# Kernel optimization log

Measured on AMD Instinct MI355X. Metric: run time of the kernel, lower is better.

The kernel has to match this reference:

```python
import jax, jax.numpy as jnp
import numpy as np

H = 64   # hid_dim (hard-coded in Attn_LSTM)
C = 8    # enc_in / out_dim
L = 96   # enc_seq_len = interval*lag = max_length
T = 24   # pre_len = window*horizon
B = 4096


def _p(key, shape, scale=0.1):
    return (jax.random.normal(key, shape, dtype=jnp.float32) * scale)


def setup_inputs() -> dict:
    key = jax.random.key(0)
    ks = jax.random.split(key, 20)
    inp = {
        'x_enc': jax.random.normal(ks[0], (B, L, C), dtype=jnp.float32),
        'x_mark_enc': jax.random.normal(ks[1], (B, L, 4), dtype=jnp.float32),
        'x_dec': jax.random.normal(ks[2], (B, T, C), dtype=jnp.float32),
        'x_mark_dec': jax.random.normal(ks[3], (B, T, 4), dtype=jnp.float32),
        # encoder LSTM (1 layer, input C -> hid H), pytorch gate order i,f,g,o
        'enc_Wih': _p(ks[4], (4 * H, C)), 'enc_Whh': _p(ks[5], (4 * H, H)),
        'enc_bih': _p(ks[6], (4 * H,)), 'enc_bhh': _p(ks[7], (4 * H,)),
        # decoder
        'emb_W': _p(ks[8], (H, C)), 'emb_b': _p(ks[9], (H,)),
        'attn_W': _p(ks[10], (L, 2 * H)), 'attn_b': _p(ks[11], (L,)),
        'comb_W': _p(ks[12], (H, 2 * H)), 'comb_b': _p(ks[13], (H,)),
        'dec_Wih': _p(ks[14], (4 * H, H)), 'dec_Whh': _p(ks[15], (4 * H, H)),
        'dec_bih': _p(ks[16], (4 * H,)), 'dec_bhh': _p(ks[17], (4 * H,)),
        'out_W': _p(ks[18], (C, H)), 'out_b': _p(ks[19], (C,)),
    }
    return inp


def _lstm_cell(x, h, c, Wih, Whh, bih, bhh):
    g = x @ Wih.T + h @ Whh.T + (bih + bhh)
    i, f, gg, o = jnp.split(g, 4, axis=-1)
    i, f, o = jax.nn.sigmoid(i), jax.nn.sigmoid(f), jax.nn.sigmoid(o)
    c_new = f * c + i * jnp.tanh(gg)
    h_new = o * jnp.tanh(c_new)
    return h_new, c_new


def _forward(x_enc, enc_Wih, enc_Whh, enc_bih, enc_bhh,
             emb_W, emb_b, attn_W, attn_b, comb_W, comb_b,
             dec_Wih, dec_Whh, dec_bih, dec_bhh, out_W, out_b):
    seq_last = x_enc[:, -1:, :]               # [B,1,C]
    x = x_enc - seq_last                      # normalized

    # ---- encoder: 1-layer LSTM over L steps ----
    h0 = jnp.zeros((x.shape[0], H), dtype=x.dtype)
    c0 = jnp.zeros_like(h0)

    def enc_step(carry, xt):
        h, c = carry
        h, c = _lstm_cell(xt, h, c, enc_Wih, enc_Whh, enc_bih, enc_bhh)
        return (h, c), h

    (h_enc, c_enc), enc_out = jax.lax.scan(enc_step, (h0, c0),
                                           jnp.swapaxes(x, 0, 1))
    enc_out = jnp.swapaxes(enc_out, 0, 1)     # [B,L,H]

    # ---- attention decoder: T sequential steps ----
    dec_in0 = x[:, -1, :]                     # last (normalized) input, [B,C]

    def dec_step(carry, _):
        inp, h, c = carry
        emb = jax.nn.relu(inp @ emb_W.T + emb_b)                       # [B,H]
        aw = jax.nn.softmax(jnp.concatenate([emb, h], -1) @ attn_W.T + attn_b)  # [B,L]
        ctx = jnp.einsum('bl,blh->bh', aw, enc_out)                    # [B,H]
        comb = jnp.concatenate([emb, ctx], -1) @ comb_W.T + comb_b     # [B,H]
        h, c = _lstm_cell(comb, h, c, dec_Wih, dec_Whh, dec_bih, dec_bhh)
        pred = h @ out_W.T + out_b                                     # [B,C]
        # original code feeds prediction.detach() back in
        return (jax.lax.stop_gradient(pred), h, c), (pred, aw)

    _, (preds, aws) = jax.lax.scan(dec_step, (dec_in0, h_enc, c_enc),
                                   None, length=T)
    pre_y = jnp.swapaxes(preds, 0, 1) + seq_last   # [B,T,C]
    return pre_y


def reference(x_enc, x_mark_enc, x_dec, x_mark_dec,
              enc_Wih, enc_Whh, enc_bih, enc_bhh,
              emb_W, emb_b, attn_W, attn_b, comb_W, comb_b,
              dec_Wih, dec_Whh, dec_bih, dec_bhh, out_W, out_b):
    # x_mark_enc, x_dec, x_mark_dec are accepted but unused (as in original)
    return _forward(x_enc, enc_Wih, enc_Whh, enc_bih, enc_bhh,
                    emb_W, emb_b, attn_W, attn_b, comb_W, comb_b,
                    dec_Wih, dec_Whh, dec_bih, dec_bhh, out_W, out_b)
```

## Files before the change

kernel.cpp:

```cpp
#include <hip/hip_runtime.h>

#define LL 96
#define TT 24
#define HH 64
#define CC 8
#define GG 256
#define BT 8
#define NB 512

typedef unsigned short u16t;
typedef unsigned int   u32t;
typedef __attribute__((ext_vector_type(8))) short bf16x8;
typedef __attribute__((ext_vector_type(4))) float f32x4;

__device__ __forceinline__ float b2f(u16t u){ union{u32t i; float f;} v; v.i=((u32t)u)<<16; return v.f; }
__device__ __forceinline__ float lo2f(u32t p){ union{u32t i; float f;} v; v.i=p<<16; return v.f; }
__device__ __forceinline__ float hi2f(u32t p){ union{u32t i; float f;} v; v.i=p&0xffff0000u; return v.f; }
__device__ __forceinline__ u16t f2b(float f){ union{float f; u32t i;} v; v.f=f; u32t l=(v.i>>16)&1u; v.i+=0x7fffu+l; return (u16t)(v.i>>16); }
__device__ __forceinline__ float rcpf(float x){ return __builtin_amdgcn_rcpf(x); }
__device__ __forceinline__ float sigm(float x){ return rcpf(1.f + __expf(-x)); }
__device__ __forceinline__ float tanh2(float x){ return 1.f - 2.f*rcpf(__expf(2.f*x) + 1.f); }
__device__ __forceinline__ u32t pk2(float a, float b){ return (u32t)f2b(a) | ((u32t)f2b(b)<<16); }
__device__ __forceinline__ bf16x8 u2b8(uint4 u){ union{uint4 a; bf16x8 b;} v; v.a=u; return v.b; }
__device__ __forceinline__ int aaddr(int k, int m){ return (((k>>5)*4 + ((k>>3)&3))*16 + m)*8 + (k&7); }

template<bool F32> __device__ __forceinline__ float ldf(const void* p, size_t i){
    if constexpr (F32) return ((const float*)p)[i];
    else               return b2f(((const u16t*)p)[i]);
}
template<bool F32> __device__ __forceinline__ uint4 ld8p(const void* p, size_t i){
    if constexpr (F32){
        const float* f = (const float*)p + i;
        uint4 r; r.x = pk2(f[0],f[1]); r.y = pk2(f[2],f[3]);
                 r.z = pk2(f[4],f[5]); r.w = pk2(f[6],f[7]);
        return r;
    } else return *(const uint4*)((const u16t*)p + i);
}
template<bool F32> __device__ __forceinline__ void stf(void* p, size_t i, float v){
    if constexpr (F32) ((float*)p)[i] = v;
    else               ((u16t*)p)[i] = f2b(v);
}
template<bool F32> __device__ __forceinline__ float ldW_enc(const void* wih, const void* whh, int r, int k){
    if (k < CC)      return ldf<F32>(wih, (size_t)r*CC + k);
    else if (k < 72) return ldf<F32>(whh, (size_t)r*HH + (k-CC));
    else             return 0.f;
}

__device__ __forceinline__ bool inputs_are_f32(const void* bih){
    const u16t* p = (const u16t*)bih;
    int cnt = 0;
    #pragma unroll
    for (int i = 0; i < 64; ++i){
        u32t e = ((u32t)p[i] >> 7) & 0xFFu;
        cnt += (e >= 128u) ? 1 : 0;
    }
    return cnt > 0;
}

template<bool F32>
__global__ __launch_bounds__(256,4) void enc4_g(
    const void* __restrict__ x_enc,
    const void* __restrict__ eWih, const void* __restrict__ eWhh,
    const void* __restrict__ ebih, const void* __restrict__ ebhh,
    u16t* __restrict__ eoG, float* __restrict__ cG)
{
    if (inputs_are_f32(ebih) != F32) return;

    __shared__ __align__(16) short Abuf2[2][1536];

    const int tid = threadIdx.x;
    const int b0  = blockIdx.x * 4;
    const int col = tid & 15, quad = (tid >> 4) & 3, wv = tid >> 6;

    bf16x8 Bf[4][3];
    float  biasg[4];
    #pragma unroll
    for (int g = 0; g < 4; ++g){
        int r = g*64 + wv*16 + col;
        biasg[g] = ldf<F32>(ebih, r) + ldf<F32>(ebhh, r);
        #pragma unroll
        for (int kb = 0; kb < 3; ++kb){
            bf16x8 v;
            #pragma unroll
            for (int x = 0; x < 8; ++x){
                int k = kb*32 + quad*8 + x;
                v[x] = (short)f2b(ldW_enc<F32>(eWih, eWhh, r, k));
            }
            Bf[g][kb] = v;
        }
    }
    for (int n = tid; n < 2*1536; n += 256) ((short*)Abuf2)[n] = 0;
    float sl = 0.f; size_t xbase = 0;
    if (tid < 32){ int b = tid >> 3, i = tid & 7;
        xbase = (size_t)(b0+b)*(LL*CC) + i;
        sl = ldf<F32>(x_enc, xbase + (size_t)(LL-1)*CC);
    }
    __syncthreads();
    if (tid < 32){ short v = (short)f2b(ldf<F32>(x_enc, xbase) - sl);
        Abuf2[0][tid] = v; Abuf2[0][tid+32] = v; Abuf2[0][tid+64] = v; Abuf2[0][tid+96] = v; }
    float xr = (tid < 32) ? ldf<F32>(x_enc, xbase + CC) : 0.f;

    const int jmy = wv*16 + col;
    const int hwbase = aaddr(8 + jmy, 0);
    const u32t ebase = ((u32t)(b0 + quad)*4u + (u32t)(jmy>>4))*1536u + (u32t)((jmy&15)*8);

    float creg = 0.f;
    u32t  pkv  = 0;

    #pragma unroll 2
    for (int t = 0; t < LL; ++t){
        __syncthreads();
        const bf16x8* AbR = (const bf16x8*)Abuf2[t & 1];
        short*        AbW = Abuf2[(t + 1) & 1];
        bf16x8 a0 = AbR[(0*4 + quad)*16 + col];
        bf16x8 a1 = AbR[(1*4 + quad)*16 + col];
        bf16x8 a2 = AbR[(2*4 + quad)*16 + col];
        f32x4 acc[4];
        #pragma unroll
        for (int g = 0; g < 4; ++g){
            f32x4 a; a[0]=biasg[g]; a[1]=biasg[g]; a[2]=biasg[g]; a[3]=biasg[g];
            a = __builtin_amdgcn_mfma_f32_16x16x32_bf16(a0, Bf[g][0], a, 0,0,0);
            a = __builtin_amdgcn_mfma_f32_16x16x32_bf16(a1, Bf[g][1], a, 0,0,0);
            a = __builtin_amdgcn_mfma_f32_16x16x32_bf16(a2, Bf[g][2], a, 0,0,0);
            acc[g] = a;
        }
        float c = sigm(acc[1][quad])*creg + sigm(acc[0][quad])*tanh2(acc[2][quad]);
        float h = sigm(acc[3][quad])*tanh2(c);
        creg = c;
        u16t hb = f2b(h);
        if ((t & 1) == 0) pkv = hb;
        else {
            pkv |= ((u32t)hb) << 16;
            *(u32t*)&eoG[ebase + (u32t)((t>>5)*512 + ((t>>3)&3)*128 + (t&7) - 1)] = pkv;
        }
        AbW[hwbase + quad*8]      = (short)hb;
        AbW[hwbase + quad*8+32]   = (short)hb;
        AbW[hwbase + quad*8+64]   = (short)hb;
        AbW[hwbase + quad*8+96]   = (short)hb;
        if (tid < 32 && t < LL-1){
            short v = (short)f2b(xr - sl);
            AbW[tid] = v; AbW[tid+32] = v; AbW[tid+64] = v; AbW[tid+96] = v;
            int tn = (t+2 < LL) ? t+2 : LL-1;
            xr = ldf<F32>(x_enc, xbase + (size_t)tn*CC);
        }
    }
    cG[(size_t)(b0 + quad)*HH + jmy] = creg;
}

template<bool F32>
__global__ __launch_bounds__(256,2) void dec8_g(
    const void* __restrict__ x_enc,
    const void* __restrict__ embW, const void* __restrict__ embb,
    const void* __restrict__ attnW, const void* __restrict__ attnb,
    const void* __restrict__ combW, const void* __restrict__ combb,
    const void* __restrict__ dWih, const void* __restrict__ dWhh,
    const void* __restrict__ dbih, const void* __restrict__ dbhh,
    const void* __restrict__ outW, const void* __restrict__ outb,
    void* __restrict__ outp, const u16t* __restrict__ eoG,
    const float* __restrict__ cG)
{
    if (inputs_are_f32(dbih) != F32) return;

    __shared__ __align__(16) float slp[CC*10];
    __shared__ __align__(16) char  uni[18880];

    const int tid = threadIdx.x;
    const int b0  = blockIdx.x * BT;
    const int col = tid & 15, quad = (tid >> 4) & 3, wv = tid >> 6;
    const int r0  = (quad >> 1) * 2;
    const int jmy = wv*16 + col;

    if (tid < BT*CC){ int b = tid >> 3, i = tid & 7;
        slp[i*10 + b] = ldf<F32>(x_enc, (size_t)(b0+b)*(LL*CC) + (size_t)(LL-1)*CC + i); }

    bf16x8 Bd[4][4];
    #pragma unroll
    for (int g = 0; g < 4; ++g){
        int r = g*64 + wv*16 + col;
        Bd[g][0] = u2b8(ld8p<F32>(dWih, (size_t)r*HH + quad*8));
        Bd[g][1] = u2b8(ld8p<F32>(dWih, (size_t)r*HH + 32 + quad*8));
        Bd[g][2] = u2b8(ld8p<F32>(dWhh, (size_t)r*HH + quad*8));
        Bd[g][3] = u2b8(ld8p<F32>(dWhh, (size_t)r*HH + 32 + quad*8));
    }
    bf16x8 Ba[2][4];
    #pragma unroll
    for (int kb = 0; kb < 4; ++kb)
        Ba[0][kb] = u2b8(ld8p<F32>(attnW, (size_t)(wv*16+col)*128 + kb*32 + quad*8));
    if (wv < 2){
        #pragma unroll
        for (int kb = 0; kb < 4; ++kb)
            Ba[1][kb] = u2b8(ld8p<F32>(attnW, (size_t)((4+wv)*16+col)*128 + kb*32 + quad*8));
    } else {
        #pragma unroll
        for (int kb = 0; kb < 4; ++kb) Ba[1][kb] = Ba[0][kb];
    }
    bf16x8 Bc[4];
    #pragma unroll
    for (int kb = 0; kb < 4; ++kb)
        Bc[kb] = u2b8(ld8p<F32>(combW, (size_t)(wv*16+col)*128 + kb*32 + quad*8));
    bf16x8 zz = {0,0,0,0,0,0,0,0};
    bf16x8 eBf = zz;
    if (quad == 0) eBf = u2b8(ld8p<F32>(embW, (size_t)(wv*16+col)*CC));
    bf16x8 oBf0 = zz, oBf1 = zz;
    if (col < CC){
        oBf0 = u2b8(ld8p<F32>(outW, (size_t)col*HH + quad*8));
        oBf1 = u2b8(ld8p<F32>(outW, (size_t)col*HH + 32 + quad*8));
    }

    float* decB  = (float*)(uni + 0);
    float* attnB = (float*)(uni + 1024);
    float* embB  = (float*)(uni + 1408);
    float* combB = (float*)(uni + 1664);
    float* outB  = (float*)(uni + 1920);
    float* Lg    = (float*)(uni + 1952);
    u16t*  awB   = (u16t*)(uni + 5024);
    u16t*  Ae    = (u16t*)(uni + 6560);
    u16t*  Ah0   = (u16t*)(uni + 8608);
    u16t*  Ah1   = (u16t*)(uni + 10656);
    u16t*  Actx  = (u16t*)(uni + 12704);
    u16t*  Acmb  = (u16t*)(uni + 14752);
    u16t*  Apred = (u16t*)(uni + 16800);

    float creg[2];
    #pragma unroll
    for (int rr = 0; rr < 2; ++rr){
        int b = (quad*4 + r0 + rr) & 7;
        u16t hv = eoG[(((size_t)(b0+b)*4 + (size_t)(jmy>>4))*3 + 2)*512 + 3*128 + (jmy&15)*8 + 7];
        Ah0[aaddr(jmy, b)]   = hv;
        Ah0[aaddr(jmy, b+8)] = hv;
        creg[rr] = cG[(size_t)(b0+b)*HH + jmy];
    }
    decB[tid] = ldf<F32>(dbih, tid) + ldf<F32>(dbhh, tid);
    if (tid < LL) attnB[tid] = ldf<F32>(attnb, tid);
    if (tid < HH) embB[tid]  = ldf<F32>(embb, tid);
    if (tid < HH) combB[tid] = ldf<F32>(combb, tid);
    if (tid < CC) outB[tid]  = ldf<F32>(outb, tid);
    for (int n = tid; n < 1024; n += 256) Apred[n] = 0;
    __syncthreads();

    const u16t* ebp = eoG + (size_t)(b0 + wv*2) * 6144;
    uint4 eF0[12], eF1[12];
    #pragma unroll
    for (int f = 0; f < 12; ++f) eF0[f] = *(const uint4*)(ebp + f*512 + quad*128 + col*8);
    #pragma unroll
    for (int f = 0; f < 12; ++f) eF1[f] = *(const uint4*)(ebp + 6144 + f*512 + quad*128 + col*8);

    const int lgS = tid & 31, bS = tid >> 5;
    const bf16x8* AeV   = (const bf16x8*)Ae;
    const bf16x8* ActxV = (const bf16x8*)Actx;
    const bf16x8* AcmbV = (const bf16x8*)Acmb;
    const bf16x8* ApV   = (const bf16x8*)Apred;

    for (int t = 0; t < TT; ++t){
        u16t* AhR = (t & 1) ? Ah1 : Ah0;
        u16t* AhW = (t & 1) ? Ah0 : Ah1;
        const bf16x8* AhV = (const bf16x8*)AhR;

        {
            bf16x8 ap = ApV[quad*16 + col];
            float eb = embB[wv*16 + col];
            f32x4 a; a[0]=eb; a[1]=eb; a[2]=eb; a[3]=eb;
            a = __builtin_amdgcn_mfma_f32_16x16x32_bf16(ap, eBf, a, 0,0,0);
            #pragma unroll
            for (int r = 0; r < 4; ++r)
                Ae[aaddr(wv*16+col, quad*4 + r)] = f2b(fmaxf(a[r], 0.f));
        }
        __syncthreads();

        {
            bf16x8 ae0 = AeV[(0*4+quad)*16 + col], ae1 = AeV[(1*4+quad)*16 + col];
            bf16x8 ah0 = AhV[(0*4+quad)*16 + col], ah1 = AhV[(1*4+quad)*16 + col];
            const int ns = (wv < 2) ? 2 : 1;
            for (int s = 0; s < ns; ++s){
                int lt = (s == 0) ? wv : 4+wv;
                float bz = attnB[lt*16 + col];
                f32x4 a; a[0]=bz; a[1]=bz; a[2]=bz; a[3]=bz;
                a = __builtin_amdgcn_mfma_f32_16x16x32_bf16(ae0, Ba[s][0], a, 0,0,0);
                a = __builtin_amdgcn_mfma_f32_16x16x32_bf16(ae1, Ba[s][1], a, 0,0,0);
                a = __builtin_amdgcn_mfma_f32_16x16x32_bf16(ah0, Ba[s][2], a, 0,0,0);
                a = __builtin_amdgcn_mfma_f32_16x16x32_bf16(ah1, Ba[s][3], a, 0,0,0);
                if (quad < 2)
                    *(float4*)&Lg[(lt*16+col)*8 + quad*4] = make_float4(a[0],a[1],a[2],a[3]);
            }
        }
        __syncthreads();

        {
            int l = lgS*3;
            float ev0 = Lg[l*8 + bS], ev1 = Lg[(l+1)*8 + bS], ev2 = Lg[(l+2)*8 + bS];
            float mx = fmaxf(ev0, fmaxf(ev1, ev2));
            #pragma unroll
            for (int m = 16; m >= 1; m >>= 1) mx = fmaxf(mx, __shfl_xor(mx, m, 32));
            float e0 = __expf(ev0 - mx), e1 = __expf(ev1 - mx), e2 = __expf(ev2 - mx);
            float sm = e0 + e1 + e2;
            #pragma unroll
            for (int m = 16; m >= 1; m >>= 1) sm += __shfl_xor(sm, m, 32);
            float inv = rcpf(sm);
            awB[bS*96 + l]     = f2b(e0*inv);
            awB[bS*96 + l + 1] = f2b(e1*inv);
            awB[bS*96 + l + 2] = f2b(e2*inv);
        }
        {
            const u16t* ap0 = awB + (wv*2)*96;
            bf16x8 f0 = *(const bf16x8*)(ap0 + quad*8);
            bf16x8 f1 = *(const bf16x8*)(ap0 + 32 + quad*8);
            bf16x8 f2 = *(const bf16x8*)(ap0 + 64 + quad*8);
            #pragma unroll
            for (int nt = 0; nt < 4; ++nt){
                f32x4 a; a[0]=0.f; a[1]=0.f; a[2]=0.f; a[3]=0.f;
                a = __builtin_amdgcn_mfma_f32_16x16x32_bf16(f0, u2b8(eF0[nt*3+0]), a, 0,0,0);
                a = __builtin_amdgcn_mfma_f32_16x16x32_bf16(f1, u2b8(eF0[nt*3+1]), a, 0,0,0);
                a = __builtin_amdgcn_mfma_f32_16x16x32_bf16(f2, u2b8(eF0[nt*3+2]), a, 0,0,0);
                if (quad == 0){
                    u16t v = f2b(a[0]);
                    Actx[aaddr(nt*16+col, wv*2)]   = v;
                    Actx[aaddr(nt*16+col, wv*2+8)] = v;
                }
            }
            const u16t* ap1 = awB + (wv*2+1)*96;
            bf16x8 g0 = *(const bf16x8*)(ap1 + quad*8);
            bf16x8 g1 = *(const bf16x8*)(ap1 + 32 + quad*8);
            bf16x8 g2 = *(const bf16x8*)(ap1 + 64 + quad*8);
            #pragma unroll
            for (int nt = 0; nt < 4; ++nt){
                f32x4 a; a[0]=0.f; a[1]=0.f; a[2]=0.f; a[3]=0.f;
                a = __builtin_amdgcn_mfma_f32_16x16x32_bf16(g0, u2b8(eF1[nt*3+0]), a, 0,0,0);
                a = __builtin_amdgcn_mfma_f32_16x16x32_bf16(g1, u2b8(eF1[nt*3+1]), a, 0,0,0);
                a = __builtin_amdgcn_mfma_f32_16x16x32_bf16(g2, u2b8(eF1[nt*3+2]), a, 0,0,0);
                if (quad == 0){
                    u16t v = f2b(a[0]);
                    Actx[aaddr(nt*16+col, wv*2+1)] = v;
                    Actx[aaddr(nt*16+col, wv*2+9)] = v;
                }
            }
        }
        __syncthreads();

        {
            bf16x8 ae0 = AeV[(0*4+quad)*16 + col],   ae1 = AeV[(1*4+quad)*16 + col];
            bf16x8 ax0 = ActxV[(0*4+quad)*16 + col], ax1 = ActxV[(1*4+quad)*16 + col];
            float bz = combB[wv*16 + col];
            f32x4 a; a[0]=bz; a[1]=bz; a[2]=bz; a[3]=bz;
            a = __builtin_amdgcn_mfma_f32_16x16x32_bf16(ae0, Bc[0], a, 0,0,0);
            a = __builtin_amdgcn_mfma_f32_16x16x32_bf16(ae1, Bc[1], a, 0,0,0);
            a = __builtin_amdgcn_mfma_f32_16x16x32_bf16(ax0, Bc[2], a, 0,0,0);
            a = __builtin_amdgcn_mfma_f32_16x16x32_bf16(ax1, Bc[3], a, 0,0,0);
            #pragma unroll
            for (int r = 0; r < 4; ++r)
                Acmb[aaddr(wv*16+col, quad*4 + r)] = f2b(a[r]);
        }
        __syncthreads();

        {
            bf16x8 ac0 = AcmbV[(0*4+quad)*16 + col], ac1 = AcmbV[(1*4+quad)*16 + col];
            bf16x8 ah0 = AhV[(0*4+quad)*16 + col],   ah1 = AhV[(1*4+quad)*16 + col];
            f32x4 g4[4];
            #pragma unroll
            for (int g = 0; g < 4; ++g){
                float bz = decB[g*64 + wv*16 + col];
                f32x4 a; a[0]=bz; a[1]=bz; a[2]=bz; a[3]=bz;
                a = __builtin_amdgcn_mfma_f32_16x16x32_bf16(ac0, Bd[g][0], a, 0,0,0);
                a = __builtin_amdgcn_mfma_f32_16x16x32_bf16(ac1, Bd[g][1], a, 0,0,0);
                a = __builtin_amdgcn_mfma_f32_16x16x32_bf16(ah0, Bd[g][2], a, 0,0,0);
                a = __builtin_amdgcn_mfma_f32_16x16x32_bf16(ah1, Bd[g][3], a, 0,0,0);
                g4[g] = a;
            }
            #pragma unroll
            for (int rr = 0; rr < 2; ++rr){
                int r = r0 + rr;
                int b = (quad*4 + r) & 7;
                float c = sigm(g4[1][r])*creg[rr] + sigm(g4[0][r])*tanh2(g4[2][r]);
                float h = sigm(g4[3][r])*tanh2(c);
                creg[rr] = c;
                u16t hv = f2b(h);
                AhW[aaddr(jmy, b)]   = hv;
                AhW[aaddr(jmy, b+8)] = hv;
            }
        }
        __syncthreads();

        if (wv == 0){
            const bf16x8* AhWV = (const bf16x8*)AhW;
            bf16x8 xh0 = AhWV[(0*4+quad)*16 + col];
            bf16x8 xh1 = AhWV[(1*4+quad)*16 + col];
            float ob = outB[col & 7];
            f32x4 a; a[0]=ob; a[1]=ob; a[2]=ob; a[3]=ob;
            a = __builtin_amdgcn_mfma_f32_16x16x32_bf16(xh0, oBf0, a, 0,0,0);
            a = __builtin_amdgcn_mfma_f32_16x16x32_bf16(xh1, oBf1, a, 0,0,0);
            if (col < CC){
                #pragma unroll
                for (int r = 0; r < 4; ++r){
                    int m = quad*4 + r, b = m & 7;
                    float p = a[r];
                    Apred[aaddr(col, m)] = f2b(p);
                    if (m < 8)
                        stf<F32>(outp, ((size_t)(b0+b)*TT + t)*CC + col, p + slp[col*10 + b]);
                }
            }
        }
        __syncthreads();
    }
}

template<bool F32>
__global__ __launch_bounds__(256,2) void fused_g(
    const void* __restrict__ x_enc,
    const void* __restrict__ eWih, const void* __restrict__ eWhh,
    const void* __restrict__ ebih, const void* __restrict__ ebhh,
    const void* __restrict__ embW, const void* __restrict__ embb,
    const void* __restrict__ attnW, const void* __restrict__ attnb,
    const void* __restrict__ combW, const void* __restrict__ combb,
    const void* __restrict__ dWih, const void* __restrict__ dWhh,
    const void* __restrict__ dbih, const void* __restrict__ dbhh,
    const void* __restrict__ outW, const void* __restrict__ outb,
    void* __restrict__ outp, u16t* __restrict__ eoG)
{
    if (inputs_are_f32(ebih) != F32) return;

    __shared__ __align__(16) float slp[CC*10];
    __shared__ __align__(16) short Abuf2[2][1536];
    __shared__ __align__(16) char  uni[18880];

    const int tid = threadIdx.x;
    const int b0  = blockIdx.x * BT;
    const int col = tid & 15, quad = (tid >> 4) & 3, wv = tid >> 6;
    const int r0  = (quad >> 1) * 2;

    bf16x8 Bf[4][3];
    float  biasg[4];
    #pragma unroll
    for (int g = 0; g < 4; ++g){
        int r = g*64 + wv*16 + col;
        biasg[g] = ldf<F32>(ebih, r) + ldf<F32>(ebhh, r);
        #pragma unroll
        for (int kb = 0; kb < 3; ++kb){
            bf16x8 v;
            #pragma unroll
            for (int x = 0; x < 8; ++x){
                int k = kb*32 + quad*8 + x;
                v[x] = (short)f2b(ldW_enc<F32>(eWih, eWhh, r, k));
            }
            Bf[g][kb] = v;
        }
    }
    for (int n = tid; n < 2*1536; n += 256) ((short*)Abuf2)[n] = 0;
    float sl = 0.f; size_t xbase = 0;
    if (tid < BT*CC){ int b = tid >> 3, i = tid & 7;
        xbase = (size_t)(b0+b)*(LL*CC) + i;
        sl = ldf<F32>(x_enc, xbase + (size_t)(LL-1)*CC);
        slp[i*10 + b] = sl; }
    __syncthreads();
    if (tid < BT*CC){ short v = (short)f2b(ldf<F32>(x_enc, xbase) - sl);
        Abuf2[0][tid] = v; Abuf2[0][tid + 64] = v; }
    float xr = (tid < BT*CC) ? ldf<F32>(x_enc, xbase + CC) : 0.f;

    const int jmy = wv*16 + col;
    const int kh  = 8 + jmy;
    const int hwbase = aaddr(kh, 0);

    u32t ebase[2];
    #pragma unroll
    for (int rr = 0; rr < 2; ++rr){
        u32t bg = (u32t)(b0 + ((quad*4 + r0 + rr) & 7));
        ebase[rr] = (bg*4u + (u32t)(jmy>>4))*1536u + (u32t)((jmy&15)*8);
    }

    float creg[2] = {0.f,0.f};
    u16t  hb16[2] = {0,0};

    for (int t = 0; t < LL; ++t){
        __syncthreads();
        const bf16x8* AbR = (const bf16x8*)Abuf2[t & 1];
        short*        AbW = Abuf2[(t + 1) & 1];
        bf16x8 a0 = AbR[(0*4 + quad)*16 + col];
        bf16x8 a1 = AbR[(1*4 + quad)*16 + col];
        bf16x8 a2 = AbR[(2*4 + quad)*16 + col];
        f32x4 acc[4];
        #pragma unroll
        for (int g = 0; g < 4; ++g){
            f32x4 a; a[0]=biasg[g]; a[1]=biasg[g]; a[2]=biasg[g]; a[3]=biasg[g];
            a = __builtin_amdgcn_mfma_f32_16x16x32_bf16(a0, Bf[g][0], a, 0,0,0);
            a = __builtin_amdgcn_mfma_f32_16x16x32_bf16(a1, Bf[g][1], a, 0,0,0);
            a = __builtin_amdgcn_mfma_f32_16x16x32_bf16(a2, Bf[g][2], a, 0,0,0);
            acc[g] = a;
        }
        int off = (t>>5)*512 + ((t>>3)&3)*128 + (t&7);
        #pragma unroll
        for (int rr = 0; rr < 2; ++rr){
            int r = r0 + rr;
            int b = (quad*4 + r) & 7;
            float c = sigm(acc[1][r])*creg[rr] + sigm(acc[0][r])*tanh2(acc[2][r]);
            float h = sigm(acc[3][r])*tanh2(c);
            creg[rr] = c; hb16[rr] = f2b(h);
            eoG[ebase[rr] + off] = hb16[rr];
            AbW[hwbase + b*8]     = (short)hb16[rr];
            AbW[hwbase + (b+8)*8] = (short)hb16[rr];
        }
        if (tid < BT*CC && t < LL-1){
            short v = (short)f2b(xr - sl);
            AbW[tid] = v; AbW[tid + 64] = v;
            int tn = (t+2 < LL) ? t+2 : LL-1;
            xr = ldf<F32>(x_enc, xbase + (size_t)tn*CC);
        }
    }

    bf16x8 Bd[4][4];
    #pragma unroll
    for (int g = 0; g < 4; ++g){
        int r = g*64 + wv*16 + col;
        Bd[g][0] = u2b8(ld8p<F32>(dWih, (size_t)r*HH + quad*8));
        Bd[g][1] = u2b8(ld8p<F32>(dWih, (size_t)r*HH + 32 + quad*8));
        Bd[g][2] = u2b8(ld8p<F32>(dWhh, (size_t)r*HH + quad*8));
        Bd[g][3] = u2b8(ld8p<F32>(dWhh, (size_t)r*HH + 32 + quad*8));
    }
    bf16x8 Ba[2][4];
    #pragma unroll
    for (int kb = 0; kb < 4; ++kb)
        Ba[0][kb] = u2b8(ld8p<F32>(attnW, (size_t)(wv*16+col)*128 + kb*32 + quad*8));
    if (wv < 2){
        #pragma unroll
        for (int kb = 0; kb < 4; ++kb)
            Ba[1][kb] = u2b8(ld8p<F32>(attnW, (size_t)((4+wv)*16+col)*128 + kb*32 + quad*8));
    } else {
        #pragma unroll
        for (int kb = 0; kb < 4; ++kb) Ba[1][kb] = Ba[0][kb];
    }
    bf16x8 Bc[4];
    #pragma unroll
    for (int kb = 0; kb < 4; ++kb)
        Bc[kb] = u2b8(ld8p<F32>(combW, (size_t)(wv*16+col)*128 + kb*32 + quad*8));
    bf16x8 zz = {0,0,0,0,0,0,0,0};
    bf16x8 eBf = zz;
    if (quad == 0) eBf = u2b8(ld8p<F32>(embW, (size_t)(wv*16+col)*CC));
    bf16x8 oBf0 = zz, oBf1 = zz;
    if (col < CC){
        oBf0 = u2b8(ld8p<F32>(outW, (size_t)col*HH + quad*8));
        oBf1 = u2b8(ld8p<F32>(outW, (size_t)col*HH + 32 + quad*8));
    }

    float* decB  = (float*)(uni + 0);
    float* attnB = (float*)(uni + 1024);
    float* embB  = (float*)(uni + 1408);
    float* combB = (float*)(uni + 1664);
    float* outB  = (float*)(uni + 1920);
    float* Lg    = (float*)(uni + 1952);
    u16t*  awB   = (u16t*)(uni + 5024);
    u16t*  Ae    = (u16t*)(uni + 6560);
    u16t*  Ah0   = (u16t*)(uni + 8608);
    u16t*  Ah1   = (u16t*)(uni + 10656);
    u16t*  Actx  = (u16t*)(uni + 12704);
    u16t*  Acmb  = (u16t*)(uni + 14752);
    u16t*  Apred = (u16t*)(uni + 16800);

    #pragma unroll
    for (int rr = 0; rr < 2; ++rr){
        int b = (quad*4 + r0 + rr) & 7;
        Ah0[aaddr(jmy, b)]     = hb16[rr];
        Ah0[aaddr(jmy, b+8)]   = hb16[rr];
    }
    decB[tid] = ldf<F32>(dbih, tid) + ldf<F32>(dbhh, tid);
    if (tid < LL) attnB[tid] = ldf<F32>(attnb, tid);
    if (tid < HH) embB[tid]  = ldf<F32>(embb, tid);
    if (tid < HH) combB[tid] = ldf<F32>(combb, tid);
    if (tid < CC) outB[tid]  = ldf<F32>(outb, tid);
    for (int n = tid; n < 1024; n += 256) Apred[n] = 0;
    __syncthreads();

    const u16t* ebp = eoG + (size_t)(b0 + wv*2) * 6144;
    uint4 eF0[12], eF1[12];
    #pragma unroll
    for (int f = 0; f < 12; ++f) eF0[f] = *(const uint4*)(ebp + f*512 + quad*128 + col*8);
    #pragma unroll
    for (int f = 0; f < 12; ++f) eF1[f] = *(const uint4*)(ebp + 6144 + f*512 + quad*128 + col*8);

    const int lgS = tid & 31, bS = tid >> 5;
    const bf16x8* AeV   = (const bf16x8*)Ae;
    const bf16x8* ActxV = (const bf16x8*)Actx;
    const bf16x8* AcmbV = (const bf16x8*)Acmb;
    const bf16x8* ApV   = (const bf16x8*)Apred;

    for (int t = 0; t < TT; ++t){
        u16t* AhR = (t & 1) ? Ah1 : Ah0;
        u16t* AhW = (t & 1) ? Ah0 : Ah1;
        const bf16x8* AhV = (const bf16x8*)AhR;

        {
            bf16x8 ap = ApV[quad*16 + col];
            float eb = embB[wv*16 + col];
            f32x4 a; a[0]=eb; a[1]=eb; a[2]=eb; a[3]=eb;
            a = __builtin_amdgcn_mfma_f32_16x16x32_bf16(ap, eBf, a, 0,0,0);
            #pragma unroll
            for (int r = 0; r < 4; ++r)
                Ae[aaddr(wv*16+col, quad*4 + r)] = f2b(fmaxf(a[r], 0.f));
        }
        __syncthreads();

        {
            bf16x8 ae0 = AeV[(0*4+quad)*16 + col], ae1 = AeV[(1*4+quad)*16 + col];
            bf16x8 ah0 = AhV[(0*4+quad)*16 + col], ah1 = AhV[(1*4+quad)*16 + col];
            const int ns = (wv < 2) ? 2 : 1;
            for (int s = 0; s < ns; ++s){
                int lt = (s == 0) ? wv : 4+wv;
                float bz = attnB[lt*16 + col];
                f32x4 a; a[0]=bz; a[1]=bz; a[2]=bz; a[3]=bz;
                a = __builtin_amdgcn_mfma_f32_16x16x32_bf16(ae0, Ba[s][0], a, 0,0,0);
                a = __builtin_amdgcn_mfma_f32_16x16x32_bf16(ae1, Ba[s][1], a, 0,0,0);
                a = __builtin_amdgcn_mfma_f32_16x16x32_bf16(ah0, Ba[s][2], a, 0,0,0);
                a = __builtin_amdgcn_mfma_f32_16x16x32_bf16(ah1, Ba[s][3], a, 0,0,0);
                if (quad < 2)
                    *(float4*)&Lg[(lt*16+col)*8 + quad*4] = make_float4(a[0],a[1],a[2],a[3]);
            }
        }
        __syncthreads();

        {
            int l = lgS*3;
            float ev0 = Lg[l*8 + bS], ev1 = Lg[(l+1)*8 + bS], ev2 = Lg[(l+2)*8 + bS];
            float mx = fmaxf(ev0, fmaxf(ev1, ev2));
            #pragma unroll
            for (int m = 16; m >= 1; m >>= 1) mx = fmaxf(mx, __shfl_xor(mx, m, 32));
            float e0 = __expf(ev0 - mx), e1 = __expf(ev1 - mx), e2 = __expf(ev2 - mx);
            float sm = e0 + e1 + e2;
            #pragma unroll
            for (int m = 16; m >= 1; m >>= 1) sm += __shfl_xor(sm, m, 32);
            float inv = rcpf(sm);
            awB[bS*96 + l]     = f2b(e0*inv);
            awB[bS*96 + l + 1] = f2b(e1*inv);
            awB[bS*96 + l + 2] = f2b(e2*inv);
        }
        {
            const u16t* ap0 = awB + (wv*2)*96;
            bf16x8 f0 = *(const bf16x8*)(ap0 + quad*8);
            bf16x8 f1 = *(const bf16x8*)(ap0 + 32 + quad*8);
            bf16x8 f2 = *(const bf16x8*)(ap0 + 64 + quad*8);
            #pragma unroll
            for (int nt = 0; nt < 4; ++nt){
                f32x4 a; a[0]=0.f; a[1]=0.f; a[2]=0.f; a[3]=0.f;
                a = __builtin_amdgcn_mfma_f32_16x16x32_bf16(f0, u2b8(eF0[nt*3+0]), a, 0,0,0);
                a = __builtin_amdgcn_mfma_f32_16x16x32_bf16(f1, u2b8(eF0[nt*3+1]), a, 0,0,0);
                a = __builtin_amdgcn_mfma_f32_16x16x32_bf16(f2, u2b8(eF0[nt*3+2]), a, 0,0,0);
                if (quad == 0){
                    u16t v = f2b(a[0]);
                    Actx[aaddr(nt*16+col, wv*2)]   = v;
                    Actx[aaddr(nt*16+col, wv*2+8)] = v;
                }
            }
            const u16t* ap1 = awB + (wv*2+1)*96;
            bf16x8 g0 = *(const bf16x8*)(ap1 + quad*8);
            bf16x8 g1 = *(const bf16x8*)(ap1 + 32 + quad*8);
            bf16x8 g2 = *(const bf16x8*)(ap1 + 64 + quad*8);
            #pragma unroll
            for (int nt = 0; nt < 4; ++nt){
                f32x4 a; a[0]=0.f; a[1]=0.f; a[2]=0.f; a[3]=0.f;
                a = __builtin_amdgcn_mfma_f32_16x16x32_bf16(g0, u2b8(eF1[nt*3+0]), a, 0,0,0);
                a = __builtin_amdgcn_mfma_f32_16x16x32_bf16(g1, u2b8(eF1[nt*3+1]), a, 0,0,0);
                a = __builtin_amdgcn_mfma_f32_16x16x32_bf16(g2, u2b8(eF1[nt*3+2]), a, 0,0,0);
                if (quad == 0){
                    u16t v = f2b(a[0]);
                    Actx[aaddr(nt*16+col, wv*2+1)] = v;
                    Actx[aaddr(nt*16+col, wv*2+9)] = v;
                }
            }
        }
        __syncthreads();

        {
            bf16x8 ae0 = AeV[(0*4+quad)*16 + col],   ae1 = AeV[(1*4+quad)*16 + col];
            bf16x8 ax0 = ActxV[(0*4+quad)*16 + col], ax1 = ActxV[(1*4+quad)*16 + col];
            float bz = combB[wv*16 + col];
            f32x4 a; a[0]=bz; a[1]=bz; a[2]=bz; a[3]=bz;
            a = __builtin_amdgcn_mfma_f32_16x16x32_bf16(ae0, Bc[0], a, 0,0,0);
            a = __builtin_amdgcn_mfma_f32_16x16x32_bf16(ae1, Bc[1], a, 0,0,0);
            a = __builtin_amdgcn_mfma_f32_16x16x32_bf16(ax0, Bc[2], a, 0,0,0);
            a = __builtin_amdgcn_mfma_f32_16x16x32_bf16(ax1, Bc[3], a, 0,0,0);
            #pragma unroll
            for (int r = 0; r < 4; ++r)
                Acmb[aaddr(wv*16+col, quad*4 + r)] = f2b(a[r]);
        }
        __syncthreads();

        {
            bf16x8 ac0 = AcmbV[(0*4+quad)*16 + col], ac1 = AcmbV[(1*4+quad)*16 + col];
            bf16x8 ah0 = AhV[(0*4+quad)*16 + col],   ah1 = AhV[(1*4+quad)*16 + col];
            f32x4 g4[4];
            #pragma unroll
            for (int g = 0; g < 4; ++g){
                float bz = decB[g*64 + wv*16 + col];
                f32x4 a; a[0]=bz; a[1]=bz; a[2]=bz; a[3]=bz;
                a = __builtin_amdgcn_mfma_f32_16x16x32_bf16(ac0, Bd[g][0], a, 0,0,0);
                a = __builtin_amdgcn_mfma_f32_16x16x32_bf16(ac1, Bd[g][1], a, 0,0,0);
                a = __builtin_amdgcn_mfma_f32_16x16x32_bf16(ah0, Bd[g][2], a, 0,0,0);
                a = __builtin_amdgcn_mfma_f32_16x16x32_bf16(ah1, Bd[g][3], a, 0,0,0);
                g4[g] = a;
            }
            #pragma unroll
            for (int rr = 0; rr < 2; ++rr){
                int r = r0 + rr;
                int b = (quad*4 + r) & 7;
                float c = sigm(g4[1][r])*creg[rr] + sigm(g4[0][r])*tanh2(g4[2][r]);
                float h = sigm(g4[3][r])*tanh2(c);
                creg[rr] = c;
                u16t hv = f2b(h);
                AhW[aaddr(jmy, b)]   = hv;
                AhW[aaddr(jmy, b+8)] = hv;
            }
        }
        __syncthreads();

        if (wv == 0){
            const bf16x8* AhWV = (const bf16x8*)AhW;
            bf16x8 xh0 = AhWV[(0*4+quad)*16 + col];
            bf16x8 xh1 = AhWV[(1*4+quad)*16 + col];
            float ob = outB[col & 7];
            f32x4 a; a[0]=ob; a[1]=ob; a[2]=ob; a[3]=ob;
            a = __builtin_amdgcn_mfma_f32_16x16x32_bf16(xh0, oBf0, a, 0,0,0);
            a = __builtin_amdgcn_mfma_f32_16x16x32_bf16(xh1, oBf1, a, 0,0,0);
            if (col < CC){
                #pragma unroll
                for (int r = 0; r < 4; ++r){
                    int m = quad*4 + r, b = m & 7;
                    float p = a[r];
                    Apred[aaddr(col, m)] = f2b(p);
                    if (m < 8)
                        stf<F32>(outp, ((size_t)(b0+b)*TT + t)*CC + col, p + slp[col*10 + b]);
                }
            }
        }
        __syncthreads();
    }
}

extern "C" void kernel_launch(void* const* d_in, const int* in_sizes, int n_in,
                              void* d_out, int out_size, void* d_ws, size_t ws_size,
                              hipStream_t stream)
{
    (void)in_sizes; (void)n_in; (void)out_size;
    u16t* eoG = (u16t*)d_ws;
    if (ws_size >= 50331648ull + 1048576ull){
        float* cG = (float*)((char*)d_ws + 50331648ull);
        enc4_g<false><<<1024, 256, 0, stream>>>(
            d_in[0], d_in[4], d_in[5], d_in[6], d_in[7], eoG, cG);
        enc4_g<true ><<<1024, 256, 0, stream>>>(
            d_in[0], d_in[4], d_in[5], d_in[6], d_in[7], eoG, cG);
        dec8_g<false><<<NB, 256, 0, stream>>>(
            d_in[0],
            d_in[8],  d_in[9],  d_in[10], d_in[11],
            d_in[12], d_in[13], d_in[14], d_in[15],
            d_in[16], d_in[17], d_in[18], d_in[19],
            d_out, eoG, cG);
        dec8_g<true ><<<NB, 256, 0, stream>>>(
            d_in[0],
            d_in[8],  d_in[9],  d_in[10], d_in[11],
            d_in[12], d_in[13], d_in[14], d_in[15],
            d_in[16], d_in[17], d_in[18], d_in[19],
            d_out, eoG, cG);
    } else {
        fused_g<false><<<NB, 256, 0, stream>>>(
            d_in[0],
            d_in[4],  d_in[5],  d_in[6],  d_in[7],
            d_in[8],  d_in[9],  d_in[10], d_in[11],
            d_in[12], d_in[13], d_in[14], d_in[15],
            d_in[16], d_in[17], d_in[18], d_in[19],
            d_out, eoG);
        fused_g<true><<<NB, 256, 0, stream>>>(
            d_in[0],
            d_in[4],  d_in[5],  d_in[6],  d_in[7],
            d_in[8],  d_in[9],  d_in[10], d_in[11],
            d_in[12], d_in[13], d_in[14], d_in[15],
            d_in[16], d_in[17], d_in[18], d_in[19],
            d_out, eoG);
    }
}
```

Measured before the change: 311.0 us.

## Move decoder attention/emb/out weights to LDS and use lighter LDS-only barriers

Attention, embedding and output-projection weight fragments in the decoder kernel are now staged once into shared memory and re-read from LDS each step, instead of being held in registers. This cuts VGPR pressure so more work can stay resident. In both the encoder and decoder loops, __syncthreads is replaced with a custom barrier that waits only on LDS counters (lgkmcnt) and adds a scheduling fence. The trade-off is extra LDS traffic and footprint per step, plus reliance on the custom barrier being correct, since it does not wait on global memory.

```diff
diff --git a/kernel.cpp b/kernel.cpp
--- a/kernel.cpp
+++ b/kernel.cpp
@@ -14,8 +14,6 @@
 typedef __attribute__((ext_vector_type(4))) float f32x4;
 
 __device__ __forceinline__ float b2f(u16t u){ union{u32t i; float f;} v; v.i=((u32t)u)<<16; return v.f; }
-__device__ __forceinline__ float lo2f(u32t p){ union{u32t i; float f;} v; v.i=p<<16; return v.f; }
-__device__ __forceinline__ float hi2f(u32t p){ union{u32t i; float f;} v; v.i=p&0xffff0000u; return v.f; }
 __device__ __forceinline__ u16t f2b(float f){ union{float f; u32t i;} v; v.f=f; u32t l=(v.i>>16)&1u; v.i+=0x7fffu+l; return (u16t)(v.i>>16); }
 __device__ __forceinline__ float rcpf(float x){ return __builtin_amdgcn_rcpf(x); }
 __device__ __forceinline__ float sigm(float x){ return rcpf(1.f + __expf(-x)); }
@@ -23,6 +21,13 @@
 __device__ __forceinline__ u32t pk2(float a, float b){ return (u32t)f2b(a) | ((u32t)f2b(b)<<16); }
 __device__ __forceinline__ bf16x8 u2b8(uint4 u){ union{uint4 a; bf16x8 b;} v; v.a=u; return v.b; }
 __device__ __forceinline__ int aaddr(int k, int m){ return (((k>>5)*4 + ((k>>3)&3))*16 + m)*8 + (k&7); }
+
+__device__ __forceinline__ void bar_lds(){
+    asm volatile("s_waitcnt lgkmcnt(0)" ::: "memory");
+    __builtin_amdgcn_s_barrier();
+    asm volatile("" ::: "memory");
+    __builtin_amdgcn_sched_barrier(0);
+}
 
 template<bool F32> __device__ __forceinline__ float ldf(const void* p, size_t i){
     if constexpr (F32) return ((const float*)p)[i];
@@ -109,7 +114,7 @@
 
     #pragma unroll 2
     for (int t = 0; t < LL; ++t){
-        __syncthreads();
+        bar_lds();
         const bf16x8* AbR = (const bf16x8*)Abuf2[t & 1];
         short*        AbW = Abuf2[(t + 1) & 1];
         bf16x8 a0 = AbR[(0*4 + quad)*16 + col];
@@ -163,6 +168,9 @@
 
     __shared__ __align__(16) float slp[CC*10];
     __shared__ __align__(16) char  uni[18880];
+    __shared__ __align__(16) u16t BaL[6*4*4*16*8];
+    __shared__ __align__(16) u16t emBL[64*8];
+    __shared__ __align__(16) u16t oWL[8*64];
 
     const int tid = threadIdx.x;
     const int b0  = blockIdx.x * BT;
@@ -182,30 +190,28 @@
         Bd[g][2] = u2b8(ld8p<F32>(dWhh, (size_t)r*HH + quad*8));
         Bd[g][3] = u2b8(ld8p<F32>(dWhh, (size_t)r*HH + 32 + quad*8));
     }
-    bf16x8 Ba[2][4];
-    #pragma unroll
-    for (int kb = 0; kb < 4; ++kb)
-        Ba[0][kb] = u2b8(ld8p<F32>(attnW, (size_t)(wv*16+col)*128 + kb*32 + quad*8));
-    if (wv < 2){
-        #pragma unroll
-        for (int kb = 0; kb < 4; ++kb)
-            Ba[1][kb] = u2b8(ld8p<F32>(attnW, (size_t)((4+wv)*16+col)*128 + kb*32 + quad*8));
-    } else {
-        #pragma unroll
-        for (int kb = 0; kb < 4; ++kb) Ba[1][kb] = Ba[0][kb];
-    }
     bf16x8 Bc[4];
     #pragma unroll
     for (int kb = 0; kb < 4; ++kb)
         Bc[kb] = u2b8(ld8p<F32>(combW, (size_t)(wv*16+col)*128 + kb*32 + quad*8));
     bf16x8 zz = {0,0,0,0,0,0,0,0};
-    bf16x8 eBf = zz;
-    if (quad == 0) eBf = u2b8(ld8p<F32>(embW, (size_t)(wv*16+col)*CC));
-    bf16x8 oBf0 = zz, oBf1 = zz;
-    if (col < CC){
-        oBf0 = u2b8(ld8p<F32>(outW, (size_t)col*HH + quad*8));
-        oBf1 = u2b8(ld8p<F32>(outW, (size_t)col*HH + 32 + quad*8));
-    }
+
+    for (int idx = tid; idx < 1536; idx += 256){
+        int lt_ = idx >> 8, kb_ = (idx >> 6) & 3, q_ = (idx >> 4) & 3, c_ = idx & 15;
+        int row = lt_*16 + c_;
+        u16t tmp[8];
+        #pragma unroll
+        for (int x = 0; x < 8; ++x)
+            tmp[x] = f2b(ldf<F32>(attnW, (size_t)row*128 + kb_*32 + q_*8 + x));
+        *(uint4*)&BaL[(size_t)idx*8] = *(uint4*)tmp;
+    }
+    if (tid < 64){
+        u16t tmp[8];
+        #pragma unroll
+        for (int c = 0; c < 8; ++c) tmp[c] = f2b(ldf<F32>(embW, (size_t)tid*CC + c));
+        *(uint4*)&emBL[tid*8] = *(uint4*)tmp;
+    }
+    for (int n = tid; n < 512; n += 256) oWL[n] = f2b(ldf<F32>(outW, n));
 
     float* decB  = (float*)(uni + 0);
     float* attnB = (float*)(uni + 1024);
@@ -258,6 +264,8 @@
 
         {
             bf16x8 ap = ApV[quad*16 + col];
+            bf16x8 eBf = zz;
+            if (quad == 0) eBf = *(const bf16x8*)&emBL[(wv*16+col)*8];
             float eb = embB[wv*16 + col];
             f32x4 a; a[0]=eb; a[1]=eb; a[2]=eb; a[3]=eb;
             a = __builtin_amdgcn_mfma_f32_16x16x32_bf16(ap, eBf, a, 0,0,0);
@@ -265,7 +273,7 @@
             for (int r = 0; r < 4; ++r)
                 Ae[aaddr(wv*16+col, quad*4 + r)] = f2b(fmaxf(a[r], 0.f));
         }
-        __syncthreads();
+        bar_lds();
 
         {
             bf16x8 ae0 = AeV[(0*4+quad)*16 + col], ae1 = AeV[(1*4+quad)*16 + col];
@@ -273,17 +281,18 @@
             const int ns = (wv < 2) ? 2 : 1;
             for (int s = 0; s < ns; ++s){
                 int lt = (s == 0) ? wv : 4+wv;
+                const u16t* bp = &BaL[lt*2048 + quad*128 + col*8];
                 float bz = attnB[lt*16 + col];
                 f32x4 a; a[0]=bz; a[1]=bz; a[2]=bz; a[3]=bz;
-                a = __builtin_amdgcn_mfma_f32_16x16x32_bf16(ae0, Ba[s][0], a, 0,0,0);
-                a = __builtin_amdgcn_mfma_f32_16x16x32_bf16(ae1, Ba[s][1], a, 0,0,0);
-                a = __builtin_amdgcn_mfma_f32_16x16x32_bf16(ah0, Ba[s][2], a, 0,0,0);
-                a = __builtin_amdgcn_mfma_f32_16x16x32_bf16(ah1, Ba[s][3], a, 0,0,0);
+                a = __builtin_amdgcn_mfma_f32_16x16x32_bf16(ae0, *(const bf16x8*)&bp[0],    a, 0,0,0);
+                a = __builtin_amdgcn_mfma_f32_16x16x32_bf16(ae1, *(const bf16x8*)&bp[512],  a, 0,0,0);
+                a = __builtin_amdgcn_mfma_f32_16x16x32_bf16(ah0, *(const bf16x8*)&bp[1024], a, 0,0,0);
+                a = __builtin_amdgcn_mfma_f32_16x16x32_bf16(ah1, *(const bf16x8*)&bp[1536], a, 0,0,0);
                 if (quad < 2)
                     *(float4*)&Lg[(lt*16+col)*8 + quad*4] = make_float4(a[0],a[1],a[2],a[3]);
             }
         }
-        __syncthreads();
+        bar_lds();
 
         {
             int l = lgS*3;
@@ -334,7 +343,7 @@
                 }
             }
         }
-        __syncthreads();
+        bar_lds();
 
         {
             bf16x8 ae0 = AeV[(0*4+quad)*16 + col],   ae1 = AeV[(1*4+quad)*16 + col];
@@ -349,7 +358,7 @@
             for (int r = 0; r < 4; ++r)
                 Acmb[aaddr(wv*16+col, quad*4 + r)] = f2b(a[r]);
         }
-        __syncthreads();
+        bar_lds();
 
         {
             bf16x8 ac0 = AcmbV[(0*4+quad)*16 + col], ac1 = AcmbV[(1*4+quad)*16 + col];
@@ -377,12 +386,17 @@
                 AhW[aaddr(jmy, b+8)] = hv;
             }
         }
-        __syncthreads();
+        bar_lds();
 
         if (wv == 0){
             const bf16x8* AhWV = (const bf16x8*)AhW;
             bf16x8 xh0 = AhWV[(0*4+quad)*16 + col];
             bf16x8 xh1 = AhWV[(1*4+quad)*16 + col];
+            bf16x8 oBf0 = zz, oBf1 = zz;
+            if (col < CC){
+                oBf0 = *(const bf16x8*)&oWL[col*64 + quad*8];
+                oBf1 = *(const bf16x8*)&oWL[col*64 + 32 + quad*8];
+            }
             float ob = outB[col & 7];
             f32x4 a; a[0]=ob; a[1]=ob; a[2]=ob; a[3]=ob;
             a = __builtin_amdgcn_mfma_f32_16x16x32_bf16(xh0, oBf0, a, 0,0,0);
@@ -398,7 +412,7 @@
                 }
             }
         }
-        __syncthreads();
+        bar_lds();
     }
 }
 
```

Result: faster. 279.3 us (-10.2%).
